# Kernel tuning notes

Measured on AMD Instinct MI355X. Metric: run time of the kernel, lower is better.

The kernel has to match this reference:

```python
import jax, jax.numpy as jnp
import numpy as np

TEMPERATURE = 0.5
EPS = 1e-8  # torch CosineSimilarity eps


def setup_inputs() -> dict:
    key = jax.random.key(0)
    k1, k2 = jax.random.split(key)
    N, D = 4096, 256
    z1 = jax.random.normal(k1, (N, D), dtype=jnp.float32)
    z2 = jax.random.normal(k2, (N, D), dtype=jnp.float32)
    return {"z1": z1, "z2": z2}


def reference(z1, z2):
    N = z1.shape[0]
    z = jnp.concatenate([z1, z2], axis=0)  # [2N, D]
    # cosine similarity = normalized dot products (GEMM instead of O(N^2 D) broadcast)
    norm = jnp.linalg.norm(z, axis=-1, keepdims=True)
    zn = z / jnp.maximum(norm, EPS)
    sim = (zn @ zn.T) / TEMPERATURE  # [2N, 2N]
    # mask self-similarity on the diagonal
    idx = jnp.arange(2 * N)
    sim = jnp.where(idx[:, None] == idx[None, :], -jnp.inf, sim)
    # target[i] = (i - N) mod 2N  (arange(2N).roll(N))
    target = jnp.roll(idx, N)
    logp = jax.nn.log_softmax(sim, axis=-1)
    loss = -jnp.mean(logp[idx, target])
    return loss
```

## Files before the change

kernel.cpp:

```cpp
#include <hip/hip_runtime.h>
#include <hip/hip_cooperative_groups.h>

namespace cg = cooperative_groups;

typedef __bf16 bf16x8 __attribute__((ext_vector_type(8)));
typedef float f32x4 __attribute__((ext_vector_type(4)));

#define TWO_LOG2E 2.88539008177792681f

#define GLOADLDS16(g, l) __builtin_amdgcn_global_load_lds(                     \
    (const __attribute__((address_space(1))) void*)(g),                        \
    (__attribute__((address_space(3))) void*)(l), 16, 0, 0)

__device__ __forceinline__ unsigned f2bf(float f) {
    unsigned u = __float_as_uint(f);
    return (u + 0x7FFFu + ((u >> 16) & 1u)) >> 16;
}

__device__ __forceinline__ void phase1(const float* __restrict__ z1,
                                       const float* __restrict__ z2,
                                       unsigned short* __restrict__ zn,
                                       float* __restrict__ S,
                                       float* __restrict__ out) {
    const int tid = threadIdx.x, lane = tid & 63, wave = tid >> 6;
    for (int grp = blockIdx.x; grp < 512; grp += gridDim.x) {
        if (tid < 16) S[(grp << 4) + tid] = 0.f;
        if (grp == 0 && tid == 0) out[0] = 0.f;
#pragma unroll
        for (int r = 0; r < 4; ++r) {
            int row = (grp << 4) + (wave << 2) + r;
            const float* src = (row < 4096) ? (z1 + row * 256) : (z2 + (row - 4096) * 256);
            float4 v = ((const float4*)src)[lane];
            float ss = v.x * v.x + v.y * v.y + v.z * v.z + v.w * v.w;
#pragma unroll
            for (int m = 32; m > 0; m >>= 1) ss += __shfl_xor(ss, m, 64);
            float sc = 1.0f / fmaxf(sqrtf(ss), 1e-8f);
            uint2 w;
            w.x = f2bf(v.x * sc) | (f2bf(v.y * sc) << 16);
            w.y = f2bf(v.z * sc) | (f2bf(v.w * sc) << 16);
            *(uint2*)(zn + row * 256 + (lane << 2)) = w;
        }
    }
}

__device__ __forceinline__ void phase2(const unsigned short* __restrict__ zn,
                                       float* __restrict__ S,
                                       unsigned short* __restrict__ Bs) {
    const int tid = threadIdx.x, lane = tid & 63, wave = tid >> 6;
    const int q = lane >> 4, n16 = lane & 15;
    const int wr = wave >> 1, wc = wave & 1;
    const int G = gridDim.x;

    auto stage = [&](int colBase, int h, int buf) {
        unsigned short* base = Bs + (buf << 13);
#pragma unroll
        for (int p = 0; p < 4; ++p) {
            int s16 = (p << 8) + tid;
            int c   = s16 >> 4;
            int k8  = (s16 & 15) ^ (c & 15);
            GLOADLDS16(zn + ((colBase + c) << 8) + (h << 7) + (k8 << 3),
                       base + (s16 << 3));
        }
    };

    for (int job = blockIdx.x; job < 512; job += G) {
        const int rowBase = (job >> 3) << 7;
        const int colRun  = (job & 7) << 10;

        bf16x8 a[4][8];
#pragma unroll
        for (int rt = 0; rt < 4; ++rt)
#pragma unroll
            for (int ks = 0; ks < 8; ++ks)
                a[rt][ks] = *(const bf16x8*)(zn
                    + ((rowBase + (wr << 6) + (rt << 4) + n16) << 8)
                    + (ks << 5) + (q << 3));

        float rs[4][4];
#pragma unroll
        for (int i = 0; i < 4; ++i)
#pragma unroll
            for (int j = 0; j < 4; ++j) rs[i][j] = 0.f;

        stage(colRun, 0, 0);
        int buf = 0;

        for (int tile = 0; tile < 16; ++tile) {
            const int colBase = colRun + (tile << 6);
            f32x4 acc[4][2];
#pragma unroll
            for (int rt = 0; rt < 4; ++rt)
#pragma unroll
                for (int ct = 0; ct < 2; ++ct) acc[rt][ct] = (f32x4){0.f, 0.f, 0.f, 0.f};

#pragma unroll
            for (int h = 0; h < 2; ++h) {
                __syncthreads();
                int m = (tile << 1) + h + 1;
                if (m < 32) stage(colRun + ((m >> 1) << 6), m & 1, buf ^ 1);

                const unsigned short* bb = Bs + (buf << 13);
#pragma unroll
                for (int ksl = 0; ksl < 4; ++ksl) {
                    bf16x8 bf[2];
#pragma unroll
                    for (int ct = 0; ct < 2; ++ct) {
                        int c  = (wc << 5) + (ct << 4) + n16;
                        int k8 = ((ksl << 2) | q) ^ n16;
                        bf[ct] = *(const bf16x8*)(bb + (((c << 4) | k8) << 3));
                    }
#pragma unroll
                    for (int rt = 0; rt < 4; ++rt)
#pragma unroll
                        for (int ct = 0; ct < 2; ++ct)
                            acc[rt][ct] = __builtin_amdgcn_mfma_f32_16x16x32_bf16(
                                a[rt][(h << 2) + ksl], bf[ct], acc[rt][ct], 0, 0, 0);
                }
                buf ^= 1;
            }

#pragma unroll
            for (int rt = 0; rt < 4; ++rt)
#pragma unroll
                for (int ct = 0; ct < 2; ++ct)
#pragma unroll
                    for (int r = 0; r < 4; ++r)
                        rs[rt][r] += __builtin_amdgcn_exp2f(acc[rt][ct][r] * TWO_LOG2E);
        }

        const int base = rowBase + (wr << 6) + (q << 2);
#pragma unroll
        for (int rt = 0; rt < 4; ++rt)
#pragma unroll
            for (int r = 0; r < 4; ++r) {
                float s = rs[rt][r];
                s += __shfl_xor(s, 1, 64);
                s += __shfl_xor(s, 2, 64);
                s += __shfl_xor(s, 4, 64);
                s += __shfl_xor(s, 8, 64);
                if (n16 == 0) atomicAdd(&S[base + (rt << 4) + r], s);
            }
    }
}

__device__ __forceinline__ void phase3(const unsigned short* __restrict__ zn,
                                       const float* __restrict__ S,
                                       float* __restrict__ out,
                                       float* __restrict__ vals) {
    const int tid = threadIdx.x, lane = tid & 63, wave = tid >> 6;
    const int q = lane >> 4, n16 = lane & 15;
    const int rib = (wave << 2) + q;
    for (int grp = blockIdx.x; grp < 512; grp += gridDim.x) {
        int row = (grp << 4) + rib;
        int tar = (row + 4096) & 8191;
        float drr = 0.f, drt = 0.f;
#pragma unroll
        for (int i = 0; i < 4; ++i) {
            int k = (i << 6) + (n16 << 2);
            uint2 ur = *(const uint2*)(zn + (row << 8) + k);
            uint2 ut = *(const uint2*)(zn + (tar << 8) + k);
            float a0 = __uint_as_float(ur.x << 16),  a1 = __uint_as_float(ur.x & 0xFFFF0000u);
            float a2 = __uint_as_float(ur.y << 16),  a3 = __uint_as_float(ur.y & 0xFFFF0000u);
            float b0 = __uint_as_float(ut.x << 16),  b1 = __uint_as_float(ut.x & 0xFFFF0000u);
            float b2 = __uint_as_float(ut.y << 16),  b3 = __uint_as_float(ut.y & 0xFFFF0000u);
            drr += a0 * a0 + a1 * a1 + a2 * a2 + a3 * a3;
            drt += a0 * b0 + a1 * b1 + a2 * b2 + a3 * b3;
        }
#pragma unroll
        for (int m = 1; m <= 8; m <<= 1) {
            drr += __shfl_xor(drr, m, 64);
            drt += __shfl_xor(drt, m, 64);
        }
        __syncthreads();
        if (n16 == 0) {
            float Sv = S[row] - __builtin_amdgcn_exp2f(drr * TWO_LOG2E);
            vals[rib] = 0.693147180559945f * __builtin_amdgcn_logf(Sv) - 2.0f * drt;
        }
        __syncthreads();
        if (tid == 0) {
            float s = 0.f;
#pragma unroll
            for (int i = 0; i < 16; ++i) s += vals[i];
            atomicAdd(out, s * (1.0f / 8192.0f));
        }
    }
}

__global__ void __launch_bounds__(256, 1) ntxent_fused(
    const float* __restrict__ z1, const float* __restrict__ z2,
    unsigned short* __restrict__ zn, float* __restrict__ S, float* __restrict__ out)
{
    __shared__ __align__(16) unsigned short Bs[2][8192];
    phase1(z1, z2, zn, S, out);
    cg::this_grid().sync();
    phase2(zn, S, &Bs[0][0]);
    cg::this_grid().sync();
    phase3(zn, S, out, (float*)&Bs[0][0]);
}

__global__ void __launch_bounds__(256, 2) norm_k(
    const float* __restrict__ z1, const float* __restrict__ z2,
    unsigned short* __restrict__ zn, float* __restrict__ S, float* __restrict__ out)
{ phase1(z1, z2, zn, S, out); }

__global__ void __launch_bounds__(256, 1) simexp_k(
    const unsigned short* __restrict__ zn, float* __restrict__ S)
{
    __shared__ __align__(16) unsigned short Bs[2][8192];
    phase2(zn, S, &Bs[0][0]);
}

__global__ void __launch_bounds__(256, 2) finish_k(
    const unsigned short* __restrict__ zn, const float* __restrict__ S,
    float* __restrict__ out)
{
    __shared__ float vals[16];
    phase3(zn, S, out, vals);
}

extern "C" void kernel_launch(void* const* d_in, const int* in_sizes, int n_in,
                              void* d_out, int out_size, void* d_ws, size_t ws_size,
                              hipStream_t stream)
{
    const float* z1 = (const float*)d_in[0];
    const float* z2 = (const float*)d_in[1];
    unsigned short* zn = (unsigned short*)d_ws;
    float* S = (float*)((char*)d_ws + 8192 * 256 * sizeof(unsigned short));
    float* out = (float*)d_out;

    int dev = 0;
    hipGetDevice(&dev);
    int coopOK = 0;
    hipDeviceGetAttribute(&coopOK, hipDeviceAttributeCooperativeLaunch, dev);
    int cus = 0;
    hipDeviceGetAttribute(&cus, hipDeviceAttributeMultiprocessorCount, dev);
    int maxB = 0;
    hipOccupancyMaxActiveBlocksPerMultiprocessor(&maxB, ntxent_fused, 256, 0);

    long long cap = (long long)maxB * (long long)cus;
    int G = (cap >= 512) ? 512 : (int)cap;

    if (coopOK && G >= 128) {
        void* args[] = {(void*)&z1, (void*)&z2, (void*)&zn, (void*)&S, (void*)&out};
        hipError_t err = hipLaunchCooperativeKernel(ntxent_fused, dim3(G), dim3(256),
                                                    args, 0, stream);
        if (err == hipSuccess) return;
    }
    norm_k<<<512, 256, 0, stream>>>(z1, z2, zn, S, out);
    simexp_k<<<512, 256, 0, stream>>>(zn, S);
    finish_k<<<512, 256, 0, stream>>>(zn, S, out);
}
```

Measured before the change: 122.4 us.

## Replace cooperative fused kernel with three launches and single-wave GEMM blocks

Drops the cooperative-groups fused kernel with grid syncs and always launches three separate kernels. The similarity-exp GEMM now runs 2048 one-wave blocks of 64 rows by 512 columns. It stages 32-column K-chunks into a small LDS double buffer and uses explicit vmcnt waits instead of __syncthreads. The aim is to remove grid-barrier overhead, raise occupancy and parallelism, and cut LDS sync cost. In exchange each block reuses its A fragments over fewer columns, issues more S atomics, and pays two extra kernel-launch boundaries.

```diff
diff --git a/kernel.cpp b/kernel.cpp
--- a/kernel.cpp
+++ b/kernel.cpp
@@ -1,7 +1,4 @@
 #include <hip/hip_runtime.h>
-#include <hip/hip_cooperative_groups.h>
-
-namespace cg = cooperative_groups;
 
 typedef __bf16 bf16x8 __attribute__((ext_vector_type(8)));
 typedef float f32x4 __attribute__((ext_vector_type(4)));
@@ -17,205 +14,168 @@
     return (u + 0x7FFFu + ((u >> 16) & 1u)) >> 16;
 }
 
-__device__ __forceinline__ void phase1(const float* __restrict__ z1,
-                                       const float* __restrict__ z2,
-                                       unsigned short* __restrict__ zn,
-                                       float* __restrict__ S,
-                                       float* __restrict__ out) {
-    const int tid = threadIdx.x, lane = tid & 63, wave = tid >> 6;
-    for (int grp = blockIdx.x; grp < 512; grp += gridDim.x) {
-        if (tid < 16) S[(grp << 4) + tid] = 0.f;
-        if (grp == 0 && tid == 0) out[0] = 0.f;
+__global__ void __launch_bounds__(256) normalize_kernel(
+    const float* __restrict__ z1, const float* __restrict__ z2,
+    unsigned short* __restrict__ zn, float* __restrict__ S, float* __restrict__ out)
+{
+    if (blockIdx.x < 32) S[(blockIdx.x << 8) + threadIdx.x] = 0.f;
+    if (blockIdx.x == 32 && threadIdx.x == 0) out[0] = 0.f;
+
+    const int wave = threadIdx.x >> 6, lane = threadIdx.x & 63;
+    const int row = (blockIdx.x << 2) + wave;
+    const float* src = (row < 4096) ? (z1 + row * 256) : (z2 + (row - 4096) * 256);
+    float4 v = ((const float4*)src)[lane];
+    float ss = v.x * v.x + v.y * v.y + v.z * v.z + v.w * v.w;
 #pragma unroll
-        for (int r = 0; r < 4; ++r) {
-            int row = (grp << 4) + (wave << 2) + r;
-            const float* src = (row < 4096) ? (z1 + row * 256) : (z2 + (row - 4096) * 256);
-            float4 v = ((const float4*)src)[lane];
-            float ss = v.x * v.x + v.y * v.y + v.z * v.z + v.w * v.w;
-#pragma unroll
-            for (int m = 32; m > 0; m >>= 1) ss += __shfl_xor(ss, m, 64);
-            float sc = 1.0f / fmaxf(sqrtf(ss), 1e-8f);
-            uint2 w;
-            w.x = f2bf(v.x * sc) | (f2bf(v.y * sc) << 16);
-            w.y = f2bf(v.z * sc) | (f2bf(v.w * sc) << 16);
-            *(uint2*)(zn + row * 256 + (lane << 2)) = w;
-        }
-    }
+    for (int m = 32; m > 0; m >>= 1) ss += __shfl_xor(ss, m, 64);
+    float sc = 1.0f / fmaxf(sqrtf(ss), 1e-8f);
+    uint2 w;
+    w.x = f2bf(v.x * sc) | (f2bf(v.y * sc) << 16);
+    w.y = f2bf(v.z * sc) | (f2bf(v.w * sc) << 16);
+    *(uint2*)(zn + row * 256 + (lane << 2)) = w;
 }
 
-__device__ __forceinline__ void phase2(const unsigned short* __restrict__ zn,
-                                       float* __restrict__ S,
-                                       unsigned short* __restrict__ Bs) {
-    const int tid = threadIdx.x, lane = tid & 63, wave = tid >> 6;
+__global__ void __launch_bounds__(64, 2) simexp_kernel(
+    const unsigned short* __restrict__ zn, float* __restrict__ S)
+{
+    __shared__ __align__(16) unsigned short Bs[2][2048];
+
+    const int lane = threadIdx.x;
     const int q = lane >> 4, n16 = lane & 15;
-    const int wr = wave >> 1, wc = wave & 1;
-    const int G = gridDim.x;
+    const int job = blockIdx.x;
+    const int rowBase = (job >> 4) << 6;
+    const int colRun  = (job & 15) << 9;
 
-    auto stage = [&](int colBase, int h, int buf) {
-        unsigned short* base = Bs + (buf << 13);
+    bf16x8 a[4][8];
+#pragma unroll
+    for (int rt = 0; rt < 4; ++rt)
+#pragma unroll
+        for (int ks = 0; ks < 8; ++ks)
+            a[rt][ks] = *(const bf16x8*)(zn + ((rowBase + (rt << 4) + n16) << 8)
+                                            + (ks << 5) + (q << 3));
+
+    auto stage = [&](int m, int buf) {
+        const int cc = m >> 2, kc = m & 3;
+        const int colBase = colRun + (cc << 5);
+        unsigned short* base = &Bs[buf][0];
 #pragma unroll
         for (int p = 0; p < 4; ++p) {
-            int s16 = (p << 8) + tid;
-            int c   = s16 >> 4;
-            int k8  = (s16 & 15) ^ (c & 15);
-            GLOADLDS16(zn + ((colBase + c) << 8) + (h << 7) + (k8 << 3),
-                       base + (s16 << 3));
+            int s = (p << 6) + lane;
+            int c = s >> 3, d = s & 7;
+            int k8 = d ^ (c & 7);
+            GLOADLDS16(zn + ((colBase + c) << 8) + (kc << 6) + (k8 << 3),
+                       base + (s << 3));
         }
     };
 
-    for (int job = blockIdx.x; job < 512; job += G) {
-        const int rowBase = (job >> 3) << 7;
-        const int colRun  = (job & 7) << 10;
+    float rs[4][4];
+#pragma unroll
+    for (int i = 0; i < 4; ++i)
+#pragma unroll
+        for (int j = 0; j < 4; ++j) rs[i][j] = 0.f;
 
-        bf16x8 a[4][8];
+    stage(0, 0);
+    int buf = 0;
+
+    for (int cc = 0; cc < 16; ++cc) {
+        f32x4 acc[4][2];
 #pragma unroll
         for (int rt = 0; rt < 4; ++rt)
 #pragma unroll
-            for (int ks = 0; ks < 8; ++ks)
-                a[rt][ks] = *(const bf16x8*)(zn
-                    + ((rowBase + (wr << 6) + (rt << 4) + n16) << 8)
-                    + (ks << 5) + (q << 3));
-
-        float rs[4][4];
-#pragma unroll
-        for (int i = 0; i < 4; ++i)
-#pragma unroll
-            for (int j = 0; j < 4; ++j) rs[i][j] = 0.f;
-
-        stage(colRun, 0, 0);
-        int buf = 0;
-
-        for (int tile = 0; tile < 16; ++tile) {
-            const int colBase = colRun + (tile << 6);
-            f32x4 acc[4][2];
-#pragma unroll
-            for (int rt = 0; rt < 4; ++rt)
-#pragma unroll
-                for (int ct = 0; ct < 2; ++ct) acc[rt][ct] = (f32x4){0.f, 0.f, 0.f, 0.f};
+            for (int ct = 0; ct < 2; ++ct) acc[rt][ct] = (f32x4){0.f, 0.f, 0.f, 0.f};
 
 #pragma unroll
-            for (int h = 0; h < 2; ++h) {
-                __syncthreads();
-                int m = (tile << 1) + h + 1;
-                if (m < 32) stage(colRun + ((m >> 1) << 6), m & 1, buf ^ 1);
-
-                const unsigned short* bb = Bs + (buf << 13);
-#pragma unroll
-                for (int ksl = 0; ksl < 4; ++ksl) {
-                    bf16x8 bf[2];
-#pragma unroll
-                    for (int ct = 0; ct < 2; ++ct) {
-                        int c  = (wc << 5) + (ct << 4) + n16;
-                        int k8 = ((ksl << 2) | q) ^ n16;
-                        bf[ct] = *(const bf16x8*)(bb + (((c << 4) | k8) << 3));
-                    }
-#pragma unroll
-                    for (int rt = 0; rt < 4; ++rt)
-#pragma unroll
-                        for (int ct = 0; ct < 2; ++ct)
-                            acc[rt][ct] = __builtin_amdgcn_mfma_f32_16x16x32_bf16(
-                                a[rt][(h << 2) + ksl], bf[ct], acc[rt][ct], 0, 0, 0);
-                }
-                buf ^= 1;
+        for (int kc = 0; kc < 4; ++kc) {
+            int m = (cc << 2) + kc + 1;
+            if (m < 64) {
+                stage(m, buf ^ 1);
+                asm volatile("s_waitcnt vmcnt(4)" ::: "memory");
+            } else {
+                asm volatile("s_waitcnt vmcnt(0)" ::: "memory");
             }
 
+            const unsigned short* bb = &Bs[buf][0];
 #pragma unroll
-            for (int rt = 0; rt < 4; ++rt)
+            for (int ks = 0; ks < 2; ++ks) {
+                bf16x8 bf[2];
 #pragma unroll
-                for (int ct = 0; ct < 2; ++ct)
+                for (int ct = 0; ct < 2; ++ct) {
+                    int c  = (ct << 4) + n16;
+                    int k8 = ((ks << 2) + q) ^ (c & 7);
+                    bf[ct] = *(const bf16x8*)(bb + (((c << 3) + k8) << 3));
+                }
 #pragma unroll
-                    for (int r = 0; r < 4; ++r)
-                        rs[rt][r] += __builtin_amdgcn_exp2f(acc[rt][ct][r] * TWO_LOG2E);
+                for (int rt = 0; rt < 4; ++rt)
+#pragma unroll
+                    for (int ct = 0; ct < 2; ++ct)
+                        acc[rt][ct] = __builtin_amdgcn_mfma_f32_16x16x32_bf16(
+                            a[rt][(kc << 1) + ks], bf[ct], acc[rt][ct], 0, 0, 0);
+            }
+            buf ^= 1;
         }
 
-        const int base = rowBase + (wr << 6) + (q << 2);
 #pragma unroll
         for (int rt = 0; rt < 4; ++rt)
 #pragma unroll
-            for (int r = 0; r < 4; ++r) {
-                float s = rs[rt][r];
-                s += __shfl_xor(s, 1, 64);
-                s += __shfl_xor(s, 2, 64);
-                s += __shfl_xor(s, 4, 64);
-                s += __shfl_xor(s, 8, 64);
-                if (n16 == 0) atomicAdd(&S[base + (rt << 4) + r], s);
-            }
+            for (int ct = 0; ct < 2; ++ct)
+#pragma unroll
+                for (int r = 0; r < 4; ++r)
+                    rs[rt][r] += __builtin_amdgcn_exp2f(acc[rt][ct][r] * TWO_LOG2E);
     }
+
+#pragma unroll
+    for (int rt = 0; rt < 4; ++rt)
+#pragma unroll
+        for (int r = 0; r < 4; ++r) {
+            float s = rs[rt][r];
+            s += __shfl_xor(s, 1, 64);
+            s += __shfl_xor(s, 2, 64);
+            s += __shfl_xor(s, 4, 64);
+            s += __shfl_xor(s, 8, 64);
+            if (n16 == 0) atomicAdd(&S[rowBase + (rt << 4) + (q << 2) + r], s);
+        }
 }
 
-__device__ __forceinline__ void phase3(const unsigned short* __restrict__ zn,
-                                       const float* __restrict__ S,
-                                       float* __restrict__ out,
-                                       float* __restrict__ vals) {
-    const int tid = threadIdx.x, lane = tid & 63, wave = tid >> 6;
-    const int q = lane >> 4, n16 = lane & 15;
-    const int rib = (wave << 2) + q;
-    for (int grp = blockIdx.x; grp < 512; grp += gridDim.x) {
-        int row = (grp << 4) + rib;
-        int tar = (row + 4096) & 8191;
-        float drr = 0.f, drt = 0.f;
-#pragma unroll
-        for (int i = 0; i < 4; ++i) {
-            int k = (i << 6) + (n16 << 2);
-            uint2 ur = *(const uint2*)(zn + (row << 8) + k);
-            uint2 ut = *(const uint2*)(zn + (tar << 8) + k);
-            float a0 = __uint_as_float(ur.x << 16),  a1 = __uint_as_float(ur.x & 0xFFFF0000u);
-            float a2 = __uint_as_float(ur.y << 16),  a3 = __uint_as_float(ur.y & 0xFFFF0000u);
-            float b0 = __uint_as_float(ut.x << 16),  b1 = __uint_as_float(ut.x & 0xFFFF0000u);
-            float b2 = __uint_as_float(ut.y << 16),  b3 = __uint_as_float(ut.y & 0xFFFF0000u);
-            drr += a0 * a0 + a1 * a1 + a2 * a2 + a3 * a3;
-            drt += a0 * b0 + a1 * b1 + a2 * b2 + a3 * b3;
-        }
-#pragma unroll
-        for (int m = 1; m <= 8; m <<= 1) {
-            drr += __shfl_xor(drr, m, 64);
-            drt += __shfl_xor(drt, m, 64);
-        }
-        __syncthreads();
-        if (n16 == 0) {
-            float Sv = S[row] - __builtin_amdgcn_exp2f(drr * TWO_LOG2E);
-            vals[rib] = 0.693147180559945f * __builtin_amdgcn_logf(Sv) - 2.0f * drt;
-        }
-        __syncthreads();
-        if (tid == 0) {
-            float s = 0.f;
-#pragma unroll
-            for (int i = 0; i < 16; ++i) s += vals[i];
-            atomicAdd(out, s * (1.0f / 8192.0f));
-        }
-    }
-}
-
-__global__ void __launch_bounds__(256, 1) ntxent_fused(
-    const float* __restrict__ z1, const float* __restrict__ z2,
-    unsigned short* __restrict__ zn, float* __restrict__ S, float* __restrict__ out)
-{
-    __shared__ __align__(16) unsigned short Bs[2][8192];
-    phase1(z1, z2, zn, S, out);
-    cg::this_grid().sync();
-    phase2(zn, S, &Bs[0][0]);
-    cg::this_grid().sync();
-    phase3(zn, S, out, (float*)&Bs[0][0]);
-}
-
-__global__ void __launch_bounds__(256, 2) norm_k(
-    const float* __restrict__ z1, const float* __restrict__ z2,
-    unsigned short* __restrict__ zn, float* __restrict__ S, float* __restrict__ out)
-{ phase1(z1, z2, zn, S, out); }
-
-__global__ void __launch_bounds__(256, 1) simexp_k(
-    const unsigned short* __restrict__ zn, float* __restrict__ S)
-{
-    __shared__ __align__(16) unsigned short Bs[2][8192];
-    phase2(zn, S, &Bs[0][0]);
-}
-
-__global__ void __launch_bounds__(256, 2) finish_k(
+__global__ void __launch_bounds__(256) finish_kernel(
     const unsigned short* __restrict__ zn, const float* __restrict__ S,
     float* __restrict__ out)
 {
     __shared__ float vals[16];
-    phase3(zn, S, out, vals);
+    const int tid = threadIdx.x, lane = tid & 63, wave = tid >> 6;
+    const int q = lane >> 4, n16 = lane & 15;
+    const int rib = (wave << 2) + q;
+    const int row = (blockIdx.x << 4) + rib;
+    const int tar = (row + 4096) & 8191;
+
+    float drr = 0.f, drt = 0.f;
+#pragma unroll
+    for (int i = 0; i < 4; ++i) {
+        int k = (i << 6) + (n16 << 2);
+        uint2 ur = *(const uint2*)(zn + (row << 8) + k);
+        uint2 ut = *(const uint2*)(zn + (tar << 8) + k);
+        float a0 = __uint_as_float(ur.x << 16),  a1 = __uint_as_float(ur.x & 0xFFFF0000u);
+        float a2 = __uint_as_float(ur.y << 16),  a3 = __uint_as_float(ur.y & 0xFFFF0000u);
+        float b0 = __uint_as_float(ut.x << 16),  b1 = __uint_as_float(ut.x & 0xFFFF0000u);
+        float b2 = __uint_as_float(ut.y << 16),  b3 = __uint_as_float(ut.y & 0xFFFF0000u);
+        drr += a0 * a0 + a1 * a1 + a2 * a2 + a3 * a3;
+        drt += a0 * b0 + a1 * b1 + a2 * b2 + a3 * b3;
+    }
+#pragma unroll
+    for (int m = 1; m <= 8; m <<= 1) {
+        drr += __shfl_xor(drr, m, 64);
+        drt += __shfl_xor(drt, m, 64);
+    }
+    if (n16 == 0) {
+        float Sv = S[row] - __builtin_amdgcn_exp2f(drr * TWO_LOG2E);
+        vals[rib] = 0.693147180559945f * __builtin_amdgcn_logf(Sv) - 2.0f * drt;
+    }
+    __syncthreads();
+    if (tid == 0) {
+        float s = 0.f;
+#pragma unroll
+        for (int i = 0; i < 16; ++i) s += vals[i];
+        atomicAdd(out, s * (1.0f / 8192.0f));
+    }
 }
 
 extern "C" void kernel_launch(void* const* d_in, const int* in_sizes, int n_in,
@@ -228,25 +188,7 @@
     float* S = (float*)((char*)d_ws + 8192 * 256 * sizeof(unsigned short));
     float* out = (float*)d_out;
 
-    int dev = 0;
-    hipGetDevice(&dev);
-    int coopOK = 0;
-    hipDeviceGetAttribute(&coopOK, hipDeviceAttributeCooperativeLaunch, dev);
-    int cus = 0;
-    hipDeviceGetAttribute(&cus, hipDeviceAttributeMultiprocessorCount, dev);
-    int maxB = 0;
-    hipOccupancyMaxActiveBlocksPerMultiprocessor(&maxB, ntxent_fused, 256, 0);
-
-    long long cap = (long long)maxB * (long long)cus;
-    int G = (cap >= 512) ? 512 : (int)cap;
-
-    if (coopOK && G >= 128) {
-        void* args[] = {(void*)&z1, (void*)&z2, (void*)&zn, (void*)&S, (void*)&out};
-        hipError_t err = hipLaunchCooperativeKernel(ntxent_fused, dim3(G), dim3(256),
-                                                    args, 0, stream);
-        if (err == hipSuccess) return;
-    }
-    norm_k<<<512, 256, 0, stream>>>(z1, z2, zn, S, out);
-    simexp_k<<<512, 256, 0, stream>>>(zn, S);
-    finish_k<<<512, 256, 0, stream>>>(zn, S, out);
+    normalize_kernel<<<2048, 256, 0, stream>>>(z1, z2, zn, S, out);
+    simexp_kernel<<<2048, 64, 0, stream>>>(zn, S);
+    finish_kernel<<<512, 256, 0, stream>>>(zn, S, out);
 }
```

Measured after the change: 107.1 us. 12.5% less time.
